# Performance work log

Hardware: AMD Instinct MI355X
Metric: run time of the kernel (lower is better)

Reference implementation:

```python
import jax, jax.numpy as jnp
from jax import lax
import numpy as np

T, B, IN, H = 192, 16, 256, 256


def setup_inputs() -> dict:
    key = jax.random.key(0)
    ks = jax.random.split(key, 8)
    s = 0.05  # small init scale to keep gates well-conditioned
    return {
        "x": jax.random.normal(ks[0], (T, B, IN), dtype=jnp.float32),
        # shared LSTM (PyTorch gate order i,f,g,o)
        "W_ih": jax.random.normal(ks[1], (4 * H, IN), dtype=jnp.float32) * s,
        "W_hh": jax.random.normal(ks[2], (4 * H, H), dtype=jnp.float32) * s,
        "b_lstm": jnp.zeros((4 * H,), dtype=jnp.float32),
        # additive attention: Ws: (IN+2H)->H, Us: H->1
        "Ws_w": jax.random.normal(ks[3], (H, IN + 2 * H), dtype=jnp.float32) * s,
        "Ws_b": jnp.zeros((H,), dtype=jnp.float32),
        "Us_w": jax.random.normal(ks[4], (1, H), dtype=jnp.float32) * s,
        "Us_b": jnp.zeros((1,), dtype=jnp.float32),
        # task-specific message LSTM cell: gates from concat(x_t, Rt, h_prev)
        "Wc": jax.random.normal(ks[5], (4 * H, IN + 2 * H), dtype=jnp.float32) * s,
        "bc": jnp.zeros((4 * H,), dtype=jnp.float32),
        "TASK": 0,
    }


def _lstm_gates(pre, c):
    i, f, g, o = jnp.split(pre, 4, axis=-1)
    i = jax.nn.sigmoid(i)
    f = jax.nn.sigmoid(f)
    g = jnp.tanh(g)
    o = jax.nn.sigmoid(o)
    c_new = f * c + i * g
    h_new = o * jnp.tanh(c_new)
    return h_new, c_new


def reference(x, W_ih, W_hh, b_lstm, Ws_w, Ws_b, Us_w, Us_b, Wc, bc, TASK):
    t_len, b, _ = x.shape
    h = W_hh.shape[1]

    h0 = jnp.zeros((b, h), x.dtype)

    # ---- shared LSTM over time ----
    def shared_step(carry, xt):
        hh, cc = carry
        pre = xt @ W_ih.T + hh @ W_hh.T + b_lstm
        hh, cc = _lstm_gates(pre, cc)
        return (hh, cc), hh

    (_, _), hs = lax.scan(shared_step, (h0, h0), x)  # hs: [T,B,H]

    # ---- per-timestep additive attention + message LSTM cell ----
    def task_step(carry, xt):
        hh, cc = carry
        h_task = jnp.broadcast_to(hh[None], (t_len, b, h))
        cat = jnp.concatenate([hs, h_task, x], axis=-1)          # [T,B,IN+2H]
        score = jnp.tanh(cat @ Ws_w.T + Ws_b) @ Us_w.T + Us_b    # [T,B,1]
        att = jax.nn.softmax(score, axis=0)                       # over time
        Rt = jnp.sum(att * hs, axis=0)                            # [B,H]
        pre = jnp.concatenate([xt, Rt, hh], axis=-1) @ Wc.T + bc
        hh, cc = _lstm_gates(pre, cc)
        return (hh, cc), hh

    (_, _), outs = lax.scan(task_step, (h0, h0), x)  # [T,B,H]
    return jnp.transpose(outs, (1, 0, 2))  # [B,T,H] (torch.stack axis=1)
```

## Files before the change

kernel.cpp:

```cpp
#include <hip/hip_runtime.h>
#include <hip/hip_fp16.h>

#define T_LEN 192

typedef unsigned long long u64;
typedef _Float16 f16x8 __attribute__((ext_vector_type(8)));
typedef float f32x4 __attribute__((ext_vector_type(4)));

#define OFF_X1F   0
#define OFF_XPRE  3145728
#define OFF_XB3   6291456
#define OFF_HSB   7077888
#define OFF_P     7864320
#define OFF_H     7921664
#define OFF_HX    7929856
#define OFF_HP    7946240
#define EXCH_WORDS 147456

#define SMEM_TASK 148736

__device__ __forceinline__ unsigned packh2(float a, float b){
  union { __half2 h; unsigned u; } v;
  v.h = __halves2half2(__float2half(a), __float2half(b));
  return v.u;
}
__device__ __forceinline__ float2 unp2(unsigned u){
  union { unsigned u32; __half2 h; } v; v.u32 = u;
  return __half22float2(v.h);
}
__device__ __forceinline__ float fdot2(unsigned a, unsigned b, float c){
#if __has_builtin(__builtin_amdgcn_fdot2)
  typedef _Float16 h2t __attribute__((ext_vector_type(2)));
  union { unsigned u; h2t h; } ua, ub;
  ua.u = a; ub.u = b;
  return __builtin_amdgcn_fdot2(ua.h, ub.h, c, false);
#else
  float2 x = unp2(a), y = unp2(b);
  return c + x.x*y.x + x.y*y.y;
#endif
}
__device__ __forceinline__ float tanh_f(float x){
  float cx = fminf(fmaxf(x, -15.f), 15.f);
  float e = __expf(2.f * cx);
  return (e - 1.f) / (e + 1.f);
}
__device__ __forceinline__ float sigm(float x){
  float cx = fminf(fmaxf(x, -30.f), 30.f);
  return 1.f / (1.f + __expf(-cx));
}

__device__ __forceinline__ u64 gld64(const u64* p){
  return __hip_atomic_load(p, __ATOMIC_RELAXED, __HIP_MEMORY_SCOPE_AGENT);
}
__device__ __forceinline__ void gst64(u64* p, u64 v){
  __hip_atomic_store(p, v, __ATOMIC_RELAXED, __HIP_MEMORY_SCOPE_AGENT);
}

__global__ __launch_bounds__(256) void initk(float* p, int n){
  int i = blockIdx.x * blockDim.x + threadIdx.x;
  int stride = gridDim.x * blockDim.x;
  for (; i < n; i += stride) p[i] = 0.f;
}

__global__ __launch_bounds__(256) void proj3(const float* __restrict__ x,
                                             const float* __restrict__ W_ih,
                                             const float* __restrict__ b_l,
                                             const float* __restrict__ Wc,
                                             const float* __restrict__ bc,
                                             const float* __restrict__ Ws_w,
                                             const float* __restrict__ Ws_b,
                                             float* __restrict__ ws){
  __shared__ float As[16 * 258];
  __shared__ float Wsh[256 * 34];
  const int bx = blockIdx.x, t = blockIdx.y, tid = threadIdx.x;
  const float* W; const float* bias; int ldw, woff, c0, mode; float* out;
  if (bx < 32)      { W = W_ih; bias = b_l;  ldw = 256; woff = 0;   c0 = bx * 32;        mode = 0; out = ws + OFF_X1F; }
  else if (bx < 64) { W = Wc;   bias = bc;   ldw = 768; woff = 0;   c0 = (bx - 32) * 32; mode = 1; out = ws + OFF_XPRE; }
  else              { W = Ws_w; bias = Ws_b; ldw = 768; woff = 512; c0 = (bx - 64) * 32; mode = 2; out = ws + OFF_XB3; }

  for (int i = 0; i < 16; ++i)
    As[i * 258 + tid] = x[(t * 16 + i) * 256 + tid];
  for (int i = 0; i < 32; ++i)
    Wsh[tid * 34 + i] = W[(c0 + i) * ldw + woff + tid];
  __syncthreads();

  const int r = tid >> 4;
  const int c2 = (tid & 15) * 2;
  float acc0 = 0.f, acc1 = 0.f;
  for (int k = 0; k < 256; k += 2) {
    float2 a  = *(const float2*)&As[r * 258 + k];
    float2 w0 = *(const float2*)&Wsh[k * 34 + c2];
    float2 w1 = *(const float2*)&Wsh[(k + 1) * 34 + c2];
    acc0 = fmaf(a.x, w0.x, acc0); acc0 = fmaf(a.y, w1.x, acc0);
    acc1 = fmaf(a.x, w0.y, acc1); acc1 = fmaf(a.y, w1.y, acc1);
  }
  const int cg = c0 + c2;
  acc0 += bias[cg]; acc1 += bias[cg + 1];
  float2 res; res.x = acc0; res.y = acc1;
  if (mode == 0) {
    *(float2*)&out[((t * 64 + (cg >> 4)) * 16 + r) * 16 + (cg & 15)] = res;
  } else if (mode == 1) {
    *(float2*)&out[(t * 16 + r) * 1024 + cg] = res;
  } else {
    *(float2*)&out[(t * 16 + r) * 256 + cg] = res;
  }
}

__global__ __launch_bounds__(512) void lstm_kernel(const float* __restrict__ X1F,
                                                   const float* __restrict__ W_hh,
                                                   float* __restrict__ hsB,
                                                   u64* __restrict__ hx){
  __shared__ unsigned hT[16 * 136];
  const int tid = threadIdx.x;
  const int wg = blockIdx.x;
  const int wave = tid >> 6, lane = tid & 63;
  const int b16 = lane & 15, quad = lane >> 4;
  const int jb = wg * 8 + wave;
  const int jpbase = (1 - wg) * 64;

  f16x8 wf[4][8];
  #pragma unroll
  for (int g = 0; g < 4; ++g) {
    #pragma unroll
    for (int kk = 0; kk < 8; ++kk) {
      int row = g * 256 + jb * 16 + b16;
      const float* wp = &W_hh[row * 256 + kk * 32 + quad * 8];
      f16x8 v;
      #pragma unroll
      for (int j = 0; j < 8; ++j) v[j] = (_Float16)wp[j];
      wf[g][kk] = v;
    }
  }
  for (int i = tid; i < 16 * 136; i += 512) hT[i] = 0u;
  float cst[4] = {0.f, 0.f, 0.f, 0.f};
  __syncthreads();

  for (int t = 0; t < T_LEN; ++t) {
    float4 xi[4];
    #pragma unroll
    for (int g = 0; g < 4; ++g)
      xi[g] = *(const float4*)&X1F[((t * 64 + g * 16 + jb) * 16 + b16) * 16 + quad * 4];

    if (t > 0) {
      const u64* src = &hx[((u64)((t - 1) & 1) * 128) * 16];
      #pragma unroll
      for (int cc = 0; cc < 2; ++cc) {
        int idx = tid * 2 + cc;
        int jpp = idx >> 4, bbq = idx & 15;
        int jp = jpbase + jpp;
        u64 v;
        do { v = gld64(&src[jp * 16 + bbq]); } while ((unsigned)v != (unsigned)t);
        hT[bbq * 136 + jp] = (unsigned)(v >> 32);
      }
    }
    __syncthreads();

    f32x4 acc[4];
    #pragma unroll
    for (int g = 0; g < 4; ++g) {
      f32x4 a; a[0]=xi[g].x; a[1]=xi[g].y; a[2]=xi[g].z; a[3]=xi[g].w;
      acc[g] = a;
    }
    #pragma unroll
    for (int kk = 0; kk < 8; ++kk) {
      union { uint4 u; f16x8 h; } bv;
      bv.u = *(const uint4*)&hT[b16 * 136 + kk * 16 + quad * 4];
      #pragma unroll
      for (int g = 0; g < 4; ++g)
        acc[g] = __builtin_amdgcn_mfma_f32_16x16x32_f16(wf[g][kk], bv.h, acc[g], 0, 0, 0);
    }
    __syncthreads();

    float hv[4];
    #pragma unroll
    for (int r = 0; r < 4; ++r) {
      float pi = acc[0][r], pf = acc[1][r], pg = acc[2][r], po = acc[3][r];
      float cn = fmaf(sigm(pf), cst[r], sigm(pi) * tanh_f(pg));
      hv[r] = sigm(po) * tanh_f(cn);
      cst[r] = cn;
    }
    int j0 = jb * 16 + quad * 4;
    int jp = j0 >> 1;
    unsigned p01 = packh2(hv[0], hv[1]);
    unsigned p23 = packh2(hv[2], hv[3]);
    u64* dst = &hx[((u64)(t & 1) * 128) * 16];
    gst64(&dst[(jp)     * 16 + b16], ((u64)p01 << 32) | (unsigned)(t + 1));
    gst64(&dst[(jp + 1) * 16 + b16], ((u64)p23 << 32) | (unsigned)(t + 1));
    *(float4*)&hsB[(b16 * 192 + t) * 256 + j0] = make_float4(hv[0], hv[1], hv[2], hv[3]);
    hT[b16 * 136 + jp]     = p01;
    hT[b16 * 136 + jp + 1] = p23;
  }
}

__global__ __launch_bounds__(1024) void task_kernel(
    const float* __restrict__ xb3, const float* __restrict__ xpre,
    const float* __restrict__ hsB, const float* __restrict__ Us_w,
    const float* __restrict__ Us_b, const float* __restrict__ Wc,
    const float* __restrict__ Ws_w,
    u64* __restrict__ Pbuf, u64* __restrict__ Hbuf, u64* __restrict__ HPbuf,
    float* __restrict__ out){
  extern __shared__ char smem[];
  unsigned* hsL  = (unsigned*)smem;
  unsigned* Ws1L = (unsigned*)(smem + 99072);
  float*    baseS= (float*)(smem + 115584);
  unsigned* WcH  = (unsigned*)smem;
  unsigned* Ws2P = (unsigned*)(smem + 65536);
  float* prel    = (float*)(smem + 82944);
  float* eel     = (float*)(smem + 89600);
  unsigned* h2l  = (unsigned*)(smem + 90368);
  unsigned* h2own= (unsigned*)(smem + 90880);
  float* hterml  = (float*)(smem + 90944);
  float* usl     = (float*)(smem + 91072);
  float* msc     = (float*)(smem + 91200);
  unsigned* G2   = (unsigned*)(smem + 99072);

  const int tid = threadIdx.x;
  const int bb = blockIdx.x & 15;
  const int s  = blockIdx.x >> 4;

  for (int idx = tid; idx < 24576; idx += 1024) {
    int tp = idx >> 7, k2 = idx & 127;
    const float* hp = &hsB[(bb * 192 + tp) * 256 + 2 * k2];
    hsL[tp * 129 + k2] = packh2(hp[0], hp[1]);
  }
  for (int idx = tid; idx < 4096; idx += 1024) {
    int c = idx >> 7, k2 = idx & 127;
    const float* wp = &Ws_w[(32 * s + c) * 768 + 2 * k2];
    Ws1L[c * 129 + k2] = packh2(wp[0], wp[1]);
  }
  __syncthreads();
  {
    int c = tid & 31, g = tid >> 5;
    float a6[6];
    #pragma unroll
    for (int j = 0; j < 6; ++j)
      a6[j] = xb3[((g * 6 + j) * 16 + bb) * 256 + 32 * s + c];
    for (int k2 = 0; k2 < 128; ++k2) {
      unsigned wv = Ws1L[c * 129 + k2];
      #pragma unroll
      for (int j = 0; j < 6; ++j)
        a6[j] = fdot2(wv, hsL[(g * 6 + j) * 129 + k2], a6[j]);
    }
    #pragma unroll
    for (int j = 0; j < 6; ++j)
      baseS[(g * 6 + j) * 33 + c] = a6[j];
  }
  __syncthreads();
  unsigned bs4[4] = {0u, 0u, 0u, 0u};
  if (tid < 768) {
    int tp = tid >> 2, q = tid & 3;
    #pragma unroll
    for (int j2 = 0; j2 < 4; ++j2)
      bs4[j2] = packh2(baseS[tp * 33 + q * 8 + 2 * j2],
                       baseS[tp * 33 + q * 8 + 2 * j2 + 1]);
  }
  __syncthreads();
  {
    int l = tid & 127, tg = tid >> 7;
    int row = (l >> 5) * 256 + 32 * s + (l & 31);
    const float* wr = &Wc[row * 768 + 256];
    float acc[24];
    #pragma unroll
    for (int i = 0; i < 24; ++i) acc[i] = 0.f;
    for (int kc = 0; kc < 128; kc += 16) {
      unsigned wv[16];
      #pragma unroll
      for (int i = 0; i < 16; ++i) {
        float2 wp2 = *(const float2*)&wr[2 * (kc + i)];
        wv[i] = packh2(wp2.x, wp2.y);
      }
      #pragma unroll
      for (int tt = 0; tt < 24; ++tt) {
        const unsigned* hp = &hsL[(tg * 24 + tt) * 129 + kc];
        float a = acc[tt];
        #pragma unroll
        for (int i = 0; i < 16; ++i) a = fdot2(wv[i], hp[i], a);
        acc[tt] = a;
      }
    }
    #pragma unroll
    for (int i = 0; i < 12; ++i)
      G2[l * 97 + tg * 12 + i] = packh2(acc[2 * i], acc[2 * i + 1]);
  }
  __syncthreads();
  for (int idx = tid; idx < 16384; idx += 1024) {
    int j = idx & 3, l = (idx >> 2) & 127, k2q = idx >> 9;
    int k2 = k2q * 4 + j;
    int row = (l >> 5) * 256 + 32 * s + (l & 31);
    const float* wp = &Wc[row * 768 + 512 + 2 * k2];
    WcH[idx] = packh2(wp[0], wp[1]);
  }
  for (int idx = tid; idx < 4096; idx += 1024) {
    int c = idx >> 4, j = idx & 15;
    const float* wp = &Ws_w[c * 768 + 256 + 2 * (16 * s + j)];
    Ws2P[c * 17 + j] = packh2(wp[0], wp[1]);
  }
  if (tid < 32) usl[tid] = Us_w[32 * s + tid];
  const float usb = Us_b[0];
  __syncthreads();

  u64* Pb  = Pbuf + (bb * 8) * 192;
  u64* Hb  = Hbuf + bb * 256;
  u64* HPb = HPbuf + (bb * 8) * 256;
  const uint4* wp4 = (const uint4*)WcH;
  const uint4* av4 = (const uint4*)h2l;
  float creg = 0.f;

  for (int t = 0; t < T_LEN; ++t) {
    const unsigned seq = (unsigned)(t + 1);
    float xp0 = 0.f, xp1 = 0.f, xp2 = 0.f, xp3 = 0.f;
    if (tid < 32) {
      const float* xq = &xpre[(t * 16 + bb) * 1024 + 32 * s + tid];
      xp0 = xq[0]; xp1 = xq[256]; xp2 = xq[512]; xp3 = xq[768];
    }
    if (t > 0) {
      if (tid < 256) {
        int c = tid >> 3, sp = tid & 7;
        u64 v;
        do { v = gld64(&HPb[sp * 256 + 32 * s + c]); } while ((unsigned)v != (unsigned)t);
        float a = __uint_as_float((unsigned)(v >> 32));
        a += __shfl_xor(a, 1); a += __shfl_xor(a, 2); a += __shfl_xor(a, 4);
        if (sp == 0) hterml[c] = a;
      } else if (tid < 512) {
        int col = tid - 256;
        u64 v;
        do { v = gld64(&Hb[col]); } while ((unsigned)v != (unsigned)t);
        float hvv = __uint_as_float((unsigned)(v >> 32));
        float hp_ = __shfl_xor(hvv, 1);
        if ((col & 1) == 0) h2l[col >> 1] = packh2(hvv, hp_);
      }
    } else {
      if (tid < 32) hterml[tid] = 0.f;
      if (tid < 128) h2l[tid] = 0u;
    }
    __syncthreads();
    if (tid < 768) {
      int tp = tid >> 2, q = tid & 3;
      float p = 0.f;
      #pragma unroll
      for (int m = 0; m < 4; ++m) {
        float2 bv = unp2(bs4[m]);
        int c0 = q * 8 + 2 * m;
        p += usl[c0]     * tanh_f(bv.x + hterml[c0]);
        p += usl[c0 + 1] * tanh_f(bv.y + hterml[c0 + 1]);
      }
      p += __shfl_xor(p, 1);
      p += __shfl_xor(p, 2);
      if ((tid & 3) == 0)
        gst64(&Pb[s * 192 + tp], ((u64)__float_as_uint(p) << 32) | seq);
    }
    {
      int l = tid & 127, kq = tid >> 7;
      float a = 0.f;
      #pragma unroll
      for (int i = 0; i < 4; ++i) {
        uint4 w4 = wp4[(kq * 4 + i) * 128 + l];
        uint4 a4 = av4[kq * 4 + i];
        a = fdot2(w4.x, a4.x, a); a = fdot2(w4.y, a4.y, a);
        a = fdot2(w4.z, a4.z, a); a = fdot2(w4.w, a4.w, a);
      }
      prel[l * 13 + kq] = a;
    }
    if (tid < 192) {
      u64 v[8];
      for (;;) {
        bool ok = true;
        #pragma unroll
        for (int sp = 0; sp < 8; ++sp) {
          v[sp] = gld64(&Pb[sp * 192 + tid]);
          ok &= ((unsigned)v[sp] == seq);
        }
        if (ok) break;
      }
      float sum = 0.f;
      #pragma unroll
      for (int sp = 0; sp < 8; ++sp) sum += __uint_as_float((unsigned)(v[sp] >> 32));
      eel[tid] = __expf(sum + usb);
    }
    __syncthreads();
    if (tid < 64) {
      float aa = eel[tid] + eel[tid + 64] + eel[tid + 128];
      #pragma unroll
      for (int off = 32; off >= 1; off >>= 1) aa += __shfl_xor(aa, off);
      if (tid == 0) msc[0] = 1.f / aa;
    }
    if (tid >= 512) {
      int l = (tid - 512) & 127, tq = (tid - 512) >> 7;
      const unsigned* gp = &G2[l * 97 + tq * 24];
      const float2* ep = (const float2*)&eel[tq * 48];
      float a = 0.f;
      #pragma unroll
      for (int i = 0; i < 24; ++i) {
        float2 g = unp2(gp[i]);
        float2 e = ep[i];
        a = fmaf(g.x, e.x, a); a = fmaf(g.y, e.y, a);
      }
      prel[l * 13 + 8 + tq] = a;
    }
    __syncthreads();
    if (tid < 32) {
      float m = msc[0];
      float pr[4];
      #pragma unroll
      for (int g = 0; g < 4; ++g) {
        const float* pp = &prel[(g * 32 + tid) * 13];
        float hsum = pp[0] + pp[1] + pp[2] + pp[3] + pp[4] + pp[5] + pp[6] + pp[7];
        float gsum = pp[8] + pp[9] + pp[10] + pp[11];
        pr[g] = hsum + m * gsum;
      }
      pr[0] += xp0; pr[1] += xp1; pr[2] += xp2; pr[3] += xp3;
      float cn = fmaf(sigm(pr[1]), creg, sigm(pr[0]) * tanh_f(pr[2]));
      float hh = sigm(pr[3]) * tanh_f(cn);
      creg = cn;
      gst64(&Hb[32 * s + tid], ((u64)__float_as_uint(hh) << 32) | seq);
      out[(bb * 192 + t) * 256 + 32 * s + tid] = hh;
      float hp_ = __shfl_xor(hh, 1);
      if ((tid & 1) == 0) h2own[tid >> 1] = packh2(hh, hp_);
    }
    __syncthreads();
    if (tid < 256) {
      float a = 0.f;
      const unsigned* wp = &Ws2P[tid * 17];
      #pragma unroll
      for (int j = 0; j < 16; ++j) a = fdot2(wp[j], h2own[j], a);
      gst64(&HPb[s * 256 + tid], ((u64)__float_as_uint(a) << 32) | seq);
    }
  }
}

extern "C" void kernel_launch(void* const* d_in, const int* in_sizes, int n_in,
                              void* d_out, int out_size, void* d_ws, size_t ws_size,
                              hipStream_t stream) {
  (void)in_sizes; (void)n_in; (void)out_size; (void)ws_size;
  const float* x    = (const float*)d_in[0];
  const float* W_ih = (const float*)d_in[1];
  const float* W_hh = (const float*)d_in[2];
  const float* b_l  = (const float*)d_in[3];
  const float* Ws_w = (const float*)d_in[4];
  const float* Ws_b = (const float*)d_in[5];
  const float* Us_w = (const float*)d_in[6];
  const float* Us_b = (const float*)d_in[7];
  const float* Wc   = (const float*)d_in[8];
  const float* bc   = (const float*)d_in[9];
  float* out = (float*)d_out;
  float* ws = (float*)d_ws;

  hipFuncSetAttribute((const void*)task_kernel,
                      hipFuncAttributeMaxDynamicSharedMemorySize, 160 * 1024);

  initk<<<64, 256, 0, stream>>>(ws + OFF_P, EXCH_WORDS);

  proj3<<<dim3(72, 192), 256, 0, stream>>>(x, W_ih, b_l, Wc, bc, Ws_w, Ws_b, ws);

  lstm_kernel<<<2, 512, 0, stream>>>(ws + OFF_X1F, W_hh, ws + OFF_HSB,
                                     (u64*)(ws + OFF_HX));

  task_kernel<<<128, 1024, SMEM_TASK, stream>>>(
      ws + OFF_XB3, ws + OFF_XPRE, ws + OFF_HSB, Us_w, Us_b, Wc, Ws_w,
      (u64*)(ws + OFF_P), (u64*)(ws + OFF_H), (u64*)(ws + OFF_HP), out);
}
```

Before: 1.713 ms.

## Use split-fp16 MFMA for input projections and relayout exchange buffers

New measurement: 2.663 ms. 1.56x slower.

```diff
diff --git a/kernel.cpp b/kernel.cpp
--- a/kernel.cpp
+++ b/kernel.cpp
@@ -62,47 +62,77 @@
   for (; i < n; i += stride) p[i] = 0.f;
 }
 
-__global__ __launch_bounds__(256) void proj3(const float* __restrict__ x,
-                                             const float* __restrict__ W_ih,
-                                             const float* __restrict__ b_l,
-                                             const float* __restrict__ Wc,
-                                             const float* __restrict__ bc,
-                                             const float* __restrict__ Ws_w,
-                                             const float* __restrict__ Ws_b,
-                                             float* __restrict__ ws){
-  __shared__ float As[16 * 258];
-  __shared__ float Wsh[256 * 34];
+__global__ __launch_bounds__(256) void proj3m(const float* __restrict__ x,
+                                              const float* __restrict__ W_ih,
+                                              const float* __restrict__ b_l,
+                                              const float* __restrict__ Wc,
+                                              const float* __restrict__ bc,
+                                              const float* __restrict__ Ws_w,
+                                              const float* __restrict__ Ws_b,
+                                              float* __restrict__ ws){
+  __shared__ unsigned xhi[16 * 136];
+  __shared__ unsigned xlo[16 * 136];
   const int bx = blockIdx.x, t = blockIdx.y, tid = threadIdx.x;
-  const float* W; const float* bias; int ldw, woff, c0, mode; float* out;
-  if (bx < 32)      { W = W_ih; bias = b_l;  ldw = 256; woff = 0;   c0 = bx * 32;        mode = 0; out = ws + OFF_X1F; }
-  else if (bx < 64) { W = Wc;   bias = bc;   ldw = 768; woff = 0;   c0 = (bx - 32) * 32; mode = 1; out = ws + OFF_XPRE; }
-  else              { W = Ws_w; bias = Ws_b; ldw = 768; woff = 512; c0 = (bx - 64) * 32; mode = 2; out = ws + OFF_XB3; }
-
-  for (int i = 0; i < 16; ++i)
-    As[i * 258 + tid] = x[(t * 16 + i) * 256 + tid];
-  for (int i = 0; i < 32; ++i)
-    Wsh[tid * 34 + i] = W[(c0 + i) * ldw + woff + tid];
-  __syncthreads();
-
-  const int r = tid >> 4;
-  const int c2 = (tid & 15) * 2;
-  float acc0 = 0.f, acc1 = 0.f;
-  for (int k = 0; k < 256; k += 2) {
-    float2 a  = *(const float2*)&As[r * 258 + k];
-    float2 w0 = *(const float2*)&Wsh[k * 34 + c2];
-    float2 w1 = *(const float2*)&Wsh[(k + 1) * 34 + c2];
-    acc0 = fmaf(a.x, w0.x, acc0); acc0 = fmaf(a.y, w1.x, acc0);
-    acc1 = fmaf(a.x, w0.y, acc1); acc1 = fmaf(a.y, w1.y, acc1);
-  }
-  const int cg = c0 + c2;
-  acc0 += bias[cg]; acc1 += bias[cg + 1];
-  float2 res; res.x = acc0; res.y = acc1;
+
+  {
+    int row = tid >> 4, c0 = (tid & 15) * 16;
+    const float* xp = &x[(t * 16 + row) * 256 + c0];
+    #pragma unroll
+    for (int i = 0; i < 8; ++i) {
+      float2 v = *(const float2*)&xp[2 * i];
+      _Float16 h0 = (_Float16)v.x, h1 = (_Float16)v.y;
+      float l0 = v.x - (float)h0, l1 = v.y - (float)h1;
+      union { _Float16 h[2]; unsigned u; } ph, pl;
+      ph.h[0] = h0; ph.h[1] = h1;
+      pl.h[0] = (_Float16)l0; pl.h[1] = (_Float16)l1;
+      xhi[row * 136 + c0 / 2 + i] = ph.u;
+      xlo[row * 136 + c0 / 2 + i] = pl.u;
+    }
+  }
+
+  const int wave = tid >> 6, lane = tid & 63;
+  const int b16 = lane & 15, quad = lane >> 4;
+  const int n0 = bx * 64 + wave * 16;
+  const float* wrow; const float* bias; int nb, mode;
+  if (bx < 16)      { nb = n0;        wrow = &W_ih[(nb + b16) * 256];       bias = b_l;  mode = 0; }
+  else if (bx < 32) { nb = n0 - 1024; wrow = &Wc[(nb + b16) * 768];         bias = bc;   mode = 1; }
+  else              { nb = n0 - 2048; wrow = &Ws_w[(nb + b16) * 768 + 512]; bias = Ws_b; mode = 2; }
+
+  f16x8 whi[8], wlo[8];
+  #pragma unroll
+  for (int kk = 0; kk < 8; ++kk) {
+    const float* wp = wrow + kk * 32 + quad * 8;
+    f16x8 h, l;
+    #pragma unroll
+    for (int j = 0; j < 8; ++j) {
+      float v = wp[j];
+      _Float16 hh = (_Float16)v;
+      h[j] = hh; l[j] = (_Float16)(v - (float)hh);
+    }
+    whi[kk] = h; wlo[kk] = l;
+  }
+  f32x4 acc;
+  #pragma unroll
+  for (int r = 0; r < 4; ++r) acc[r] = bias[nb + quad * 4 + r];
+  __syncthreads();
+
+  #pragma unroll
+  for (int kk = 0; kk < 8; ++kk) {
+    union { uint4 u; f16x8 h; } bh, bl;
+    bh.u = *(const uint4*)&xhi[b16 * 136 + kk * 16 + quad * 4];
+    bl.u = *(const uint4*)&xlo[b16 * 136 + kk * 16 + quad * 4];
+    acc = __builtin_amdgcn_mfma_f32_16x16x32_f16(whi[kk], bh.h, acc, 0, 0, 0);
+    acc = __builtin_amdgcn_mfma_f32_16x16x32_f16(wlo[kk], bh.h, acc, 0, 0, 0);
+    acc = __builtin_amdgcn_mfma_f32_16x16x32_f16(whi[kk], bl.h, acc, 0, 0, 0);
+  }
+
+  float4 res; res.x = acc[0]; res.y = acc[1]; res.z = acc[2]; res.w = acc[3];
   if (mode == 0) {
-    *(float2*)&out[((t * 64 + (cg >> 4)) * 16 + r) * 16 + (cg & 15)] = res;
+    *(float4*)&ws[OFF_X1F + (((u64)t * 64 + (n0 >> 4)) * 16 + b16) * 16 + quad * 4] = res;
   } else if (mode == 1) {
-    *(float2*)&out[(t * 16 + r) * 1024 + cg] = res;
+    *(float4*)&ws[OFF_XPRE + ((u64)t * 16 + b16) * 1024 + nb + quad * 4] = res;
   } else {
-    *(float2*)&out[(t * 16 + r) * 256 + cg] = res;
+    *(float4*)&ws[OFF_XB3 + ((u64)t * 16 + b16) * 256 + nb + quad * 4] = res;
   }
 }
 
@@ -116,7 +146,7 @@
   const int wave = tid >> 6, lane = tid & 63;
   const int b16 = lane & 15, quad = lane >> 4;
   const int jb = wg * 8 + wave;
-  const int jpbase = (1 - wg) * 64;
+  const int peerbase = (1 - wg) * 64;
 
   f16x8 wf[4][8];
   #pragma unroll
@@ -142,16 +172,17 @@
       xi[g] = *(const float4*)&X1F[((t * 64 + g * 16 + jb) * 16 + b16) * 16 + quad * 4];
 
     if (t > 0) {
-      const u64* src = &hx[((u64)((t - 1) & 1) * 128) * 16];
-      #pragma unroll
-      for (int cc = 0; cc < 2; ++cc) {
-        int idx = tid * 2 + cc;
-        int jpp = idx >> 4, bbq = idx & 15;
-        int jp = jpbase + jpp;
-        u64 v;
-        do { v = gld64(&src[jp * 16 + bbq]); } while ((unsigned)v != (unsigned)t);
-        hT[bbq * 136 + jp] = (unsigned)(v >> 32);
-      }
+      const u64* src = &hx[((u64)((t - 1) & 1)) * 2048];
+      int bbq = tid >> 5, k2 = tid & 31;
+      int jp0 = peerbase + 2 * k2;
+      u64 v0, v1;
+      for (;;) {
+        v0 = gld64(&src[bbq * 128 + jp0]);
+        v1 = gld64(&src[bbq * 128 + jp0 + 1]);
+        if ((unsigned)v0 == (unsigned)t && (unsigned)v1 == (unsigned)t) break;
+      }
+      hT[bbq * 136 + jp0]     = (unsigned)(v0 >> 32);
+      hT[bbq * 136 + jp0 + 1] = (unsigned)(v1 >> 32);
     }
     __syncthreads();
 
@@ -183,9 +214,9 @@
     int jp = j0 >> 1;
     unsigned p01 = packh2(hv[0], hv[1]);
     unsigned p23 = packh2(hv[2], hv[3]);
-    u64* dst = &hx[((u64)(t & 1) * 128) * 16];
-    gst64(&dst[(jp)     * 16 + b16], ((u64)p01 << 32) | (unsigned)(t + 1));
-    gst64(&dst[(jp + 1) * 16 + b16], ((u64)p23 << 32) | (unsigned)(t + 1));
+    u64* dst = &hx[((u64)(t & 1)) * 2048];
+    gst64(&dst[b16 * 128 + jp],     ((u64)p01 << 32) | (unsigned)(t + 1));
+    gst64(&dst[b16 * 128 + jp + 1], ((u64)p23 << 32) | (unsigned)(t + 1));
     *(float4*)&hsB[(b16 * 192 + t) * 256 + j0] = make_float4(hv[0], hv[1], hv[2], hv[3]);
     hT[b16 * 136 + jp]     = p01;
     hT[b16 * 136 + jp + 1] = p23;
@@ -299,9 +330,9 @@
   const float usb = Us_b[0];
   __syncthreads();
 
-  u64* Pb  = Pbuf + (bb * 8) * 192;
+  u64* Pb  = Pbuf + (u64)bb * 1536;
   u64* Hb  = Hbuf + bb * 256;
-  u64* HPb = HPbuf + (bb * 8) * 256;
+  u64* HPb = HPbuf + (u64)bb * 2048;
   const uint4* wp4 = (const uint4*)WcH;
   const uint4* av4 = (const uint4*)h2l;
   float creg = 0.f;
@@ -317,7 +348,7 @@
       if (tid < 256) {
         int c = tid >> 3, sp = tid & 7;
         u64 v;
-        do { v = gld64(&HPb[sp * 256 + 32 * s + c]); } while ((unsigned)v != (unsigned)t);
+        do { v = gld64(&HPb[((u64)(32 * s + c)) * 8 + sp]); } while ((unsigned)v != (unsigned)t);
         float a = __uint_as_float((unsigned)(v >> 32));
         a += __shfl_xor(a, 1); a += __shfl_xor(a, 2); a += __shfl_xor(a, 4);
         if (sp == 0) hterml[c] = a;
@@ -347,7 +378,7 @@
       p += __shfl_xor(p, 1);
       p += __shfl_xor(p, 2);
       if ((tid & 3) == 0)
-        gst64(&Pb[s * 192 + tp], ((u64)__float_as_uint(p) << 32) | seq);
+        gst64(&Pb[(u64)tp * 8 + s], ((u64)__float_as_uint(p) << 32) | seq);
     }
     {
       int l = tid & 127, kq = tid >> 7;
@@ -367,7 +398,7 @@
         bool ok = true;
         #pragma unroll
         for (int sp = 0; sp < 8; ++sp) {
-          v[sp] = gld64(&Pb[sp * 192 + tid]);
+          v[sp] = gld64(&Pb[(u64)tid * 8 + sp]);
           ok &= ((unsigned)v[sp] == seq);
         }
         if (ok) break;
@@ -423,7 +454,7 @@
       const unsigned* wp = &Ws2P[tid * 17];
       #pragma unroll
       for (int j = 0; j < 16; ++j) a = fdot2(wp[j], h2own[j], a);
-      gst64(&HPb[s * 256 + tid], ((u64)__float_as_uint(a) << 32) | seq);
+      gst64(&HPb[(u64)tid * 8 + s], ((u64)__float_as_uint(a) << 32) | seq);
     }
   }
 }
@@ -450,7 +481,7 @@
 
   initk<<<64, 256, 0, stream>>>(ws + OFF_P, EXCH_WORDS);
 
-  proj3<<<dim3(72, 192), 256, 0, stream>>>(x, W_ih, b_l, Wc, bc, Ws_w, Ws_b, ws);
+  proj3m<<<dim3(36, 192), 256, 0, stream>>>(x, W_ih, b_l, Wc, bc, Ws_w, Ws_b, ws);
 
   lstm_kernel<<<2, 512, 0, stream>>>(ws + OFF_X1F, W_hh, ws + OFF_HSB,
                                      (u64*)(ws + OFF_HX));
```
